# Optimization experiments

Measured on AMD Instinct MI355X. Metric: run time of the kernel, lower is better.

Reference implementation:

```python
import jax, jax.numpy as jnp
import numpy as np

T, D_IN, D_OUT, E = 8192, 1024, 1024, 8
LN_EPS = 1e-5


def setup_inputs() -> dict:
    key = jax.random.key(0)
    k1, k2, k3 = jax.random.split(key, 3)
    x = jax.random.normal(k1, (T, D_IN), dtype=jnp.float32)
    # tokens are pre-sorted by expert; equal load => capacity = T // E per expert
    expert_frequency = jnp.full((E,), T // E, dtype=jnp.int64)
    # per-expert Linear(input_dim, output_dim) params
    W = jax.random.normal(k2, (E, D_IN, D_OUT), dtype=jnp.float32) / np.sqrt(D_IN)
    b = jax.random.normal(k3, (E, D_OUT), dtype=jnp.float32) * 0.02
    # per-expert LayerNorm(output_dim) affine params
    ln_gamma = jnp.ones((E, D_OUT), dtype=jnp.float32)
    ln_beta = jnp.zeros((E, D_OUT), dtype=jnp.float32)
    return {
        "expert_ordered_input": x,
        "expert_frequency": expert_frequency,
        "W": W,
        "b": b,
        "ln_gamma": ln_gamma,
        "ln_beta": ln_beta,
    }


def reference(expert_ordered_input, expert_frequency, W, b, ln_gamma, ln_beta):
    # Grouped-GEMM form of: split tokens by expert_frequency, apply per-expert
    # LayerBlock (Linear -> relu -> LayerNorm), then concat along token dim.
    # Frequencies are equal (capacity = T // E), so the ragged split is a reshape.
    x = expert_ordered_input
    n_tok, d_in = x.shape
    n_exp = W.shape[0]
    cap = n_tok // n_exp  # static capacity per expert
    xe = x.reshape(n_exp, cap, d_in)                       # [E, cap, d_in]
    h = jnp.einsum("ecd,edf->ecf", xe, W) + b[:, None, :]  # [E, cap, d_out]
    h = jax.nn.relu(h)
    mu = jnp.mean(h, axis=-1, keepdims=True)
    var = jnp.var(h, axis=-1, keepdims=True)
    hn = (h - mu) * jax.lax.rsqrt(var + LN_EPS)
    out = hn * ln_gamma[:, None, :] + ln_beta[:, None, :]
    return out.reshape(n_tok, -1)                          # concat over experts
```

## Files before the change

### kernel.cpp

```cpp
#include <hip/hip_runtime.h>
#include <hip/hip_bf16.h>
#include <stdint.h>

#define T_TOK 8192
#define DIN   1024
#define DOUT  1024
#define NEXP  8
#define CAP   1024
#define LN_EPS 1e-5f

#define BM 256
#define BN 128
#define BKT 64
#define ABUF (BM * BKT)
#define BBUF (BN * BKT)
#define BUFSZ (ABUF + BBUF)

typedef __attribute__((ext_vector_type(8))) short short8;
typedef __attribute__((ext_vector_type(4))) float f32x4;

__device__ __forceinline__ unsigned short f2bf(float f) {
    union { float f; unsigned int u; } v; v.f = f;
    unsigned int u = v.u;
    unsigned int r = u + 0x7FFFu + ((u >> 16) & 1u);
    return (unsigned short)(r >> 16);
}
__device__ __forceinline__ float bf2f(unsigned short h) {
    union { unsigned int u; float f; } v; v.u = ((unsigned int)h) << 16;
    return v.f;
}

__device__ __forceinline__ void gld16(void* l, const void* g) {
    __builtin_amdgcn_global_load_lds(
        (const __attribute__((address_space(1))) unsigned int*)(uintptr_t)g,
        (__attribute__((address_space(3))) unsigned int*)(uintptr_t)l,
        16, 0, 0);
}

__global__ __launch_bounds__(256) void prep_kernel(
    const float* __restrict__ X, const float* __restrict__ W,
    unsigned short* __restrict__ Xb, unsigned short* __restrict__ Wt) {
    __shared__ float tile[64][65];
    int blk = blockIdx.x;
    int tid = threadIdx.x;
    if (blk < 1024) {
        int e  = blk & 7;
        int r0 = (blk >> 3) * 8;
        size_t base = ((size_t)(e * CAP + r0)) * 256 + tid;
#pragma unroll
        for (int q = 0; q < 8; q++) {
            size_t i = base + (size_t)q * 256;
            float4 v = ((const float4*)X)[i];
            ushort4 o;
            o.x = f2bf(v.x); o.y = f2bf(v.y); o.z = f2bf(v.z); o.w = f2bf(v.w);
            ((ushort4*)Xb)[i] = o;
        }
    } else {
        int t  = blk - 1024;
        int e  = t & 7;
        int tl = t >> 3;
        int k0 = (tl >> 4) * 64;
        int n0 = (tl & 15) * 64;
        const float* Wp = W + (size_t)e * DIN * DOUT;
        unsigned short* Wtp = Wt + (size_t)e * DIN * DOUT;
        int rr = tid >> 4;
        int cc = tid & 15;
#pragma unroll
        for (int q = 0; q < 4; q++) {
            int k = rr + q * 16;
            float4 v = *(const float4*)(Wp + (size_t)(k0 + k) * DOUT + n0 + cc * 4);
            tile[k][cc * 4 + 0] = v.x;
            tile[k][cc * 4 + 1] = v.y;
            tile[k][cc * 4 + 2] = v.z;
            tile[k][cc * 4 + 3] = v.w;
        }
        __syncthreads();
#pragma unroll
        for (int q = 0; q < 4; q++) {
            int n = rr + q * 16;
            ushort4 o;
            o.x = f2bf(tile[cc * 4 + 0][n]);
            o.y = f2bf(tile[cc * 4 + 1][n]);
            o.z = f2bf(tile[cc * 4 + 2][n]);
            o.w = f2bf(tile[cc * 4 + 3][n]);
            *(ushort4*)(Wtp + (size_t)(n0 + n) * DIN + k0 + cc * 4) = o;
        }
    }
}

__global__ __launch_bounds__(512, 2) void gemm7_kernel(
    const unsigned short* __restrict__ Xb,
    const unsigned short* __restrict__ Wt,
    const float* __restrict__ Bias,
    unsigned short* __restrict__ Hb,
    float2* __restrict__ P)
{
    __shared__ unsigned short lds[3 * BUFSZ];

    int blk = blockIdx.x;
    int e   = blk & 7;
    int ni  = (blk >> 3) & 7;
    int mi  = blk >> 6;
    int m0  = mi * BM;
    int n0  = ni * BN;

    int t    = threadIdx.x;
    int wave = t >> 6;
    int lane = t & 63;
    int wm   = (wave >> 1) * 64;
    int wn   = (wave & 1) * 64;
    int lrow = lane & 15;
    int quad = lane >> 4;
    int l7   = lrow & 7;

    const unsigned short* Ag = Xb + (size_t)(e * CAP + m0) * DIN;
    const unsigned short* Bg = Wt + (size_t)e * DOUT * DIN + (size_t)n0 * DIN;

    int trow   = t >> 3;
    int kg_src = (t & 7) ^ (trow & 7);

    int aoff0 = (wm + lrow) * BKT + ((quad) ^ l7) * 8;
    int aoff1 = (wm + lrow) * BKT + ((4 + quad) ^ l7) * 8;
    int boff0 = (wn + lrow) * BKT + ((quad) ^ l7) * 8;
    int boff1 = (wn + lrow) * BKT + ((4 + quad) ^ l7) * 8;

    f32x4 acc[4][4];
#pragma unroll
    for (int i = 0; i < 4; i++)
#pragma unroll
        for (int j = 0; j < 4; j++)
            acc[i][j] = (f32x4)(0.0f);

#define STAGE_H(bb, k0, h)                                                     \
    {                                                                          \
        unsigned short* Ab_ = &lds[(bb) * BUFSZ];                              \
        unsigned short* Bb_ = &lds[(bb) * BUFSZ + ABUF];                       \
        gld16(Ab_ + (((h) * 2 + 0) * 512 + t) * 8,                             \
              Ag + (size_t)(((h) * 2 + 0) * 64 + trow) * DIN + (k0) + kg_src * 8); \
        gld16(Ab_ + (((h) * 2 + 1) * 512 + t) * 8,                             \
              Ag + (size_t)(((h) * 2 + 1) * 64 + trow) * DIN + (k0) + kg_src * 8); \
        gld16(Bb_ + ((h) * 512 + t) * 8,                                       \
              Bg + (size_t)((h) * 64 + trow) * DIN + (k0) + kg_src * 8);       \
    }

#define LOADFRAGS(bb, ao, bo)                                                  \
    {                                                                          \
        const unsigned short* Ab_ = &lds[(bb) * BUFSZ];                        \
        const unsigned short* Bb_ = &lds[(bb) * BUFSZ + ABUF];                 \
        _Pragma("unroll")                                                      \
        for (int i = 0; i < 4; i++)                                            \
            af[i] = *(const short8*)&Ab_[(ao) + i * 16 * BKT];                 \
        _Pragma("unroll")                                                      \
        for (int j = 0; j < 4; j++)                                            \
            bf[j] = *(const short8*)&Bb_[(bo) + j * 16 * BKT];                 \
    }

#define MFMA16()                                                               \
    {                                                                          \
        __builtin_amdgcn_s_setprio(1);                                         \
        _Pragma("unroll")                                                      \
        for (int i = 0; i < 4; i++)                                            \
            _Pragma("unroll")                                                  \
            for (int j = 0; j < 4; j++)                                        \
                acc[i][j] = __builtin_amdgcn_mfma_f32_16x16x32_bf16(           \
                    af[i], bf[j], acc[i][j], 0, 0, 0);                         \
        __builtin_amdgcn_s_setprio(0);                                         \
    }

#define BAR() __builtin_amdgcn_s_barrier()
#define VMW(n) asm volatile("s_waitcnt vmcnt(" #n ")" ::: "memory")

    STAGE_H(0, 0, 0);
    STAGE_H(0, 0, 1);
    STAGE_H(1, BKT, 0);
    STAGE_H(1, BKT, 1);
    VMW(6);
    BAR();

    int cur = 0, nxt = 1, fut = 2;
    for (int p = 0; p < 14; ++p) {
        int k2 = (p + 2) * BKT;
        {
            short8 af[4], bf[4];
            LOADFRAGS(cur, aoff0, boff0);
            STAGE_H(fut, k2, 0);
            BAR();
            MFMA16();
            BAR();
        }
        {
            short8 af[4], bf[4];
            LOADFRAGS(cur, aoff1, boff1);
            STAGE_H(fut, k2, 1);
            BAR();
            MFMA16();
            VMW(6);
            BAR();
        }
        int tmp = cur; cur = nxt; nxt = fut; fut = tmp;
    }
    {
        short8 af[4], bf[4];
        LOADFRAGS(cur, aoff0, boff0);
        BAR(); MFMA16(); BAR();
    }
    {
        short8 af[4], bf[4];
        LOADFRAGS(cur, aoff1, boff1);
        BAR(); MFMA16();
        VMW(0);
        BAR();
    }
    {
        short8 af[4], bf[4];
        LOADFRAGS(nxt, aoff0, boff0);
        BAR(); MFMA16(); BAR();
    }
    {
        short8 af[4], bf[4];
        LOADFRAGS(nxt, aoff1, boff1);
        BAR(); MFMA16();
    }

#undef STAGE_H
#undef LOADFRAGS
#undef MFMA16
#undef BAR
#undef VMW

    asm volatile("" ::: "memory");

    float bias[4];
#pragma unroll
    for (int j = 0; j < 4; j++)
        bias[j] = Bias[e * DOUT + n0 + wn + j * 16 + lrow];

    int tok0  = e * CAP + m0 + wm;
    int chunk = ni * 2 + (wave & 1);

#pragma unroll
    for (int i = 0; i < 4; i++) {
#pragma unroll
        for (int r = 0; r < 4; r++) {
            float s = 0.f, ss = 0.f;
#pragma unroll
            for (int j = 0; j < 4; j++) {
                float v = fmaxf(acc[i][j][r] + bias[j], 0.f);
                acc[i][j][r] = v;
                s += v;
                ss = fmaf(v, v, ss);
            }
#pragma unroll
            for (int m = 1; m <= 8; m <<= 1) {
                s  += __shfl_xor(s, m);
                ss += __shfl_xor(ss, m);
            }
            int grow = tok0 + i * 16 + quad * 4 + r;
            if (lrow == 0)
                P[(size_t)grow * 16 + chunk] = make_float2(s, ss);
#pragma unroll
            for (int j = 0; j < 4; j++) {
                int gcol = n0 + wn + j * 16 + lrow;
                Hb[(size_t)grow * DOUT + gcol] = f2bf(acc[i][j][r]);
            }
        }
    }
}

__global__ __launch_bounds__(256) void ln2_kernel(
    const unsigned short* __restrict__ Hb,
    const float2* __restrict__ P,
    const float* __restrict__ G,
    const float* __restrict__ Bt,
    float* __restrict__ Out)
{
    int blk = blockIdx.x;
    int e   = blk & 7;
    int r8  = (blk >> 3) * 8;
    int row0 = e * CAP + r8;
    int tid = threadIdx.x;
    __shared__ float sh[8][2];

    if (tid < 128) {
        int r = tid >> 4;
        float2 p = P[(size_t)(row0 + r) * 16 + (tid & 15)];
        float s = p.x, ss = p.y;
#pragma unroll
        for (int m = 1; m <= 8; m <<= 1) {
            s  += __shfl_xor(s, m);
            ss += __shfl_xor(ss, m);
        }
        if ((tid & 15) == 0) {
            float mu  = s * (1.0f / DOUT);
            float var = fmaxf(ss * (1.0f / DOUT) - mu * mu, 0.f);
            sh[r][0] = mu;
            sh[r][1] = rsqrtf(var + LN_EPS);
        }
    }
    __syncthreads();

    float4 g = ((const float4*)G)[e * 256 + tid];
    float4 b = ((const float4*)Bt)[e * 256 + tid];
#pragma unroll
    for (int r = 0; r < 8; r++) {
        float mu = sh[r][0], rs = sh[r][1];
        ushort4 hb = ((const ushort4*)Hb)[(size_t)(row0 + r) * 256 + tid];
        float4 y;
        y.x = (bf2f(hb.x) - mu) * rs * g.x + b.x;
        y.y = (bf2f(hb.y) - mu) * rs * g.y + b.y;
        y.z = (bf2f(hb.z) - mu) * rs * g.z + b.z;
        y.w = (bf2f(hb.w) - mu) * rs * g.w + b.w;
        ((float4*)Out)[(size_t)(row0 + r) * 256 + tid] = y;
    }
}

extern "C" void kernel_launch(void* const* d_in, const int* in_sizes, int n_in,
                              void* d_out, int out_size, void* d_ws, size_t ws_size,
                              hipStream_t stream) {
    const float* x  = (const float*)d_in[0];
    const float* W  = (const float*)d_in[2];
    const float* b  = (const float*)d_in[3];
    const float* g  = (const float*)d_in[4];
    const float* be = (const float*)d_in[5];
    float* out = (float*)d_out;

    const size_t WT_BYTES = (size_t)NEXP * DIN * DOUT * 2;
    const size_t XB_BYTES = (size_t)T_TOK * DIN * 2;
    const size_t P_BYTES  = (size_t)T_TOK * 16 * 8;
    const size_t HB_BYTES = (size_t)T_TOK * DOUT * 2;
    if (ws_size < WT_BYTES + XB_BYTES + P_BYTES + HB_BYTES) return;

    unsigned short* Wt = (unsigned short*)d_ws;
    unsigned short* Xb = (unsigned short*)((char*)d_ws + WT_BYTES);
    float2* P = (float2*)((char*)d_ws + WT_BYTES + XB_BYTES);
    unsigned short* Hb = (unsigned short*)((char*)d_ws + WT_BYTES + XB_BYTES + P_BYTES);

    prep_kernel<<<dim3(3072), dim3(256), 0, stream>>>(x, W, Xb, Wt);
    gemm7_kernel<<<dim3(256), dim3(512), 0, stream>>>(Xb, Wt, b, Hb, P);
    ln2_kernel<<<dim3(1024), dim3(256), 0, stream>>>(Hb, P, g, be, out);
}
```

Measured before the change: 142.7 us.

## Fuse prep, GEMM and LayerNorm into one cooperative kernel with grid syncs

Merges the three launches (bf16 conversion/transpose, grouped GEMM, LayerNorm) into one cooperative kernel of 256 blocks, with grid-wide syncs between phases. The aim is to cut launch overhead and the inter-kernel gaps. The trade-off is that the prep and LN phases now run with only 256 blocks instead of 3072 and 1024, which lowers parallelism for those memory-bound phases, and each grid sync adds its own cost.

```diff
diff --git a/kernel.cpp b/kernel.cpp
--- a/kernel.cpp
+++ b/kernel.cpp
@@ -1,6 +1,9 @@
 #include <hip/hip_runtime.h>
+#include <hip/hip_cooperative_groups.h>
 #include <hip/hip_bf16.h>
 #include <stdint.h>
+
+namespace cg = cooperative_groups;
 
 #define T_TOK 8192
 #define DIN   1024
@@ -37,99 +40,102 @@
         16, 0, 0);
 }
 
-__global__ __launch_bounds__(256) void prep_kernel(
+__global__ __launch_bounds__(512, 2) void fused_kernel(
     const float* __restrict__ X, const float* __restrict__ W,
-    unsigned short* __restrict__ Xb, unsigned short* __restrict__ Wt) {
-    __shared__ float tile[64][65];
+    const float* __restrict__ Bias,
+    const float* __restrict__ G, const float* __restrict__ Bt,
+    float* __restrict__ Out,
+    unsigned short* __restrict__ Wt, unsigned short* __restrict__ Xb,
+    float2* __restrict__ P, unsigned short* __restrict__ Hb)
+{
+    __shared__ unsigned short lds[3 * BUFSZ];
+
     int blk = blockIdx.x;
-    int tid = threadIdx.x;
-    if (blk < 1024) {
-        int e  = blk & 7;
-        int r0 = (blk >> 3) * 8;
-        size_t base = ((size_t)(e * CAP + r0)) * 256 + tid;
-#pragma unroll
-        for (int q = 0; q < 8; q++) {
-            size_t i = base + (size_t)q * 256;
+    int e   = blk & 7;
+    int t   = threadIdx.x;
+
+    {
+        int r0   = (blk >> 3) * 32;
+        int rsub = t >> 8;
+        int c4   = t & 255;
+        size_t base = ((size_t)(e * CAP + r0 + rsub)) * 256 + c4;
+#pragma unroll
+        for (int q = 0; q < 16; q++) {
+            size_t i = base + (size_t)(q * 2) * 256;
             float4 v = ((const float4*)X)[i];
             ushort4 o;
             o.x = f2bf(v.x); o.y = f2bf(v.y); o.z = f2bf(v.z); o.w = f2bf(v.w);
             ((ushort4*)Xb)[i] = o;
         }
-    } else {
-        int t  = blk - 1024;
-        int e  = t & 7;
-        int tl = t >> 3;
-        int k0 = (tl >> 4) * 64;
-        int n0 = (tl & 15) * 64;
+    }
+    {
+        float (*tile)[65] = (float (*)[65])lds;
         const float* Wp = W + (size_t)e * DIN * DOUT;
         unsigned short* Wtp = Wt + (size_t)e * DIN * DOUT;
-        int rr = tid >> 4;
-        int cc = tid & 15;
-#pragma unroll
-        for (int q = 0; q < 4; q++) {
-            int k = rr + q * 16;
-            float4 v = *(const float4*)(Wp + (size_t)(k0 + k) * DOUT + n0 + cc * 4);
-            tile[k][cc * 4 + 0] = v.x;
-            tile[k][cc * 4 + 1] = v.y;
-            tile[k][cc * 4 + 2] = v.z;
-            tile[k][cc * 4 + 3] = v.w;
-        }
-        __syncthreads();
-#pragma unroll
-        for (int q = 0; q < 4; q++) {
-            int n = rr + q * 16;
-            ushort4 o;
-            o.x = f2bf(tile[cc * 4 + 0][n]);
-            o.y = f2bf(tile[cc * 4 + 1][n]);
-            o.z = f2bf(tile[cc * 4 + 2][n]);
-            o.w = f2bf(tile[cc * 4 + 3][n]);
-            *(ushort4*)(Wtp + (size_t)(n0 + n) * DIN + k0 + cc * 4) = o;
-        }
-    }
-}
-
-__global__ __launch_bounds__(512, 2) void gemm7_kernel(
-    const unsigned short* __restrict__ Xb,
-    const unsigned short* __restrict__ Wt,
-    const float* __restrict__ Bias,
-    unsigned short* __restrict__ Hb,
-    float2* __restrict__ P)
-{
-    __shared__ unsigned short lds[3 * BUFSZ];
-
-    int blk = blockIdx.x;
-    int e   = blk & 7;
-    int ni  = (blk >> 3) & 7;
-    int mi  = blk >> 6;
-    int m0  = mi * BM;
-    int n0  = ni * BN;
-
-    int t    = threadIdx.x;
-    int wave = t >> 6;
-    int lane = t & 63;
-    int wm   = (wave >> 1) * 64;
-    int wn   = (wave & 1) * 64;
-    int lrow = lane & 15;
-    int quad = lane >> 4;
-    int l7   = lrow & 7;
-
-    const unsigned short* Ag = Xb + (size_t)(e * CAP + m0) * DIN;
-    const unsigned short* Bg = Wt + (size_t)e * DOUT * DIN + (size_t)n0 * DIN;
-
-    int trow   = t >> 3;
-    int kg_src = (t & 7) ^ (trow & 7);
-
-    int aoff0 = (wm + lrow) * BKT + ((quad) ^ l7) * 8;
-    int aoff1 = (wm + lrow) * BKT + ((4 + quad) ^ l7) * 8;
-    int boff0 = (wn + lrow) * BKT + ((quad) ^ l7) * 8;
-    int boff1 = (wn + lrow) * BKT + ((4 + quad) ^ l7) * 8;
-
-    f32x4 acc[4][4];
-#pragma unroll
-    for (int i = 0; i < 4; i++)
-#pragma unroll
-        for (int j = 0; j < 4; j++)
-            acc[i][j] = (f32x4)(0.0f);
+        int tb = (blk >> 3) * 8;
+        int rr = t >> 4;
+        int cc = t & 15;
+        for (int i = 0; i < 8; i++) {
+            int tl = tb + i;
+            int k0 = (tl >> 4) * 64;
+            int n0 = (tl & 15) * 64;
+            __syncthreads();
+#pragma unroll
+            for (int q = 0; q < 2; q++) {
+                int k = rr + q * 32;
+                float4 v = *(const float4*)(Wp + (size_t)(k0 + k) * DOUT + n0 + cc * 4);
+                tile[k][cc * 4 + 0] = v.x;
+                tile[k][cc * 4 + 1] = v.y;
+                tile[k][cc * 4 + 2] = v.z;
+                tile[k][cc * 4 + 3] = v.w;
+            }
+            __syncthreads();
+#pragma unroll
+            for (int q = 0; q < 2; q++) {
+                int n = rr + q * 32;
+                ushort4 o;
+                o.x = f2bf(tile[cc * 4 + 0][n]);
+                o.y = f2bf(tile[cc * 4 + 1][n]);
+                o.z = f2bf(tile[cc * 4 + 2][n]);
+                o.w = f2bf(tile[cc * 4 + 3][n]);
+                *(ushort4*)(Wtp + (size_t)(n0 + n) * DIN + k0 + cc * 4) = o;
+            }
+        }
+    }
+
+    cg::this_grid().sync();
+
+    {
+        int ni  = (blk >> 3) & 7;
+        int mi  = blk >> 6;
+        int m0  = mi * BM;
+        int n0  = ni * BN;
+
+        int wave = t >> 6;
+        int lane = t & 63;
+        int wm   = (wave >> 1) * 64;
+        int wn   = (wave & 1) * 64;
+        int lrow = lane & 15;
+        int quad = lane >> 4;
+        int l7   = lrow & 7;
+
+        const unsigned short* Ag = Xb + (size_t)(e * CAP + m0) * DIN;
+        const unsigned short* Bg = Wt + (size_t)e * DOUT * DIN + (size_t)n0 * DIN;
+
+        int trow   = t >> 3;
+        int kg_src = (t & 7) ^ (trow & 7);
+
+        int aoff0 = (wm + lrow) * BKT + ((quad) ^ l7) * 8;
+        int aoff1 = (wm + lrow) * BKT + ((4 + quad) ^ l7) * 8;
+        int boff0 = (wn + lrow) * BKT + ((quad) ^ l7) * 8;
+        int boff1 = (wn + lrow) * BKT + ((4 + quad) ^ l7) * 8;
+
+        f32x4 acc[4][4];
+#pragma unroll
+        for (int i = 0; i < 4; i++)
+#pragma unroll
+            for (int j = 0; j < 4; j++)
+                acc[i][j] = (f32x4)(0.0f);
 
 #define STAGE_H(bb, k0, h)                                                     \
     {                                                                          \
@@ -170,57 +176,57 @@
 #define BAR() __builtin_amdgcn_s_barrier()
 #define VMW(n) asm volatile("s_waitcnt vmcnt(" #n ")" ::: "memory")
 
-    STAGE_H(0, 0, 0);
-    STAGE_H(0, 0, 1);
-    STAGE_H(1, BKT, 0);
-    STAGE_H(1, BKT, 1);
-    VMW(6);
-    BAR();
-
-    int cur = 0, nxt = 1, fut = 2;
-    for (int p = 0; p < 14; ++p) {
-        int k2 = (p + 2) * BKT;
+        STAGE_H(0, 0, 0);
+        STAGE_H(0, 0, 1);
+        STAGE_H(1, BKT, 0);
+        STAGE_H(1, BKT, 1);
+        VMW(6);
+        BAR();
+
+        int cur = 0, nxt = 1, fut = 2;
+        for (int p = 0; p < 14; ++p) {
+            int k2 = (p + 2) * BKT;
+            {
+                short8 af[4], bf[4];
+                LOADFRAGS(cur, aoff0, boff0);
+                STAGE_H(fut, k2, 0);
+                BAR();
+                MFMA16();
+                BAR();
+            }
+            {
+                short8 af[4], bf[4];
+                LOADFRAGS(cur, aoff1, boff1);
+                STAGE_H(fut, k2, 1);
+                BAR();
+                MFMA16();
+                VMW(6);
+                BAR();
+            }
+            int tmp = cur; cur = nxt; nxt = fut; fut = tmp;
+        }
         {
             short8 af[4], bf[4];
             LOADFRAGS(cur, aoff0, boff0);
-            STAGE_H(fut, k2, 0);
-            BAR();
-            MFMA16();
-            BAR();
+            BAR(); MFMA16(); BAR();
         }
         {
             short8 af[4], bf[4];
             LOADFRAGS(cur, aoff1, boff1);
-            STAGE_H(fut, k2, 1);
+            BAR(); MFMA16();
+            VMW(0);
             BAR();
-            MFMA16();
-            VMW(6);
-            BAR();
-        }
-        int tmp = cur; cur = nxt; nxt = fut; fut = tmp;
-    }
-    {
-        short8 af[4], bf[4];
-        LOADFRAGS(cur, aoff0, boff0);
-        BAR(); MFMA16(); BAR();
-    }
-    {
-        short8 af[4], bf[4];
-        LOADFRAGS(cur, aoff1, boff1);
-        BAR(); MFMA16();
-        VMW(0);
-        BAR();
-    }
-    {
-        short8 af[4], bf[4];
-        LOADFRAGS(nxt, aoff0, boff0);
-        BAR(); MFMA16(); BAR();
-    }
-    {
-        short8 af[4], bf[4];
-        LOADFRAGS(nxt, aoff1, boff1);
-        BAR(); MFMA16();
-    }
+        }
+        {
+            short8 af[4], bf[4];
+            LOADFRAGS(nxt, aoff0, boff0);
+            BAR(); MFMA16(); BAR();
+        }
+        {
+            short8 af[4], bf[4];
+            LOADFRAGS(nxt, aoff1, boff1);
+            BAR(); MFMA16();
+        }
 
 #undef STAGE_H
 #undef LOADFRAGS
@@ -228,89 +234,86 @@
 #undef BAR
 #undef VMW
 
-    asm volatile("" ::: "memory");
-
-    float bias[4];
-#pragma unroll
-    for (int j = 0; j < 4; j++)
-        bias[j] = Bias[e * DOUT + n0 + wn + j * 16 + lrow];
-
-    int tok0  = e * CAP + m0 + wm;
-    int chunk = ni * 2 + (wave & 1);
-
-#pragma unroll
-    for (int i = 0; i < 4; i++) {
-#pragma unroll
-        for (int r = 0; r < 4; r++) {
-            float s = 0.f, ss = 0.f;
-#pragma unroll
-            for (int j = 0; j < 4; j++) {
-                float v = fmaxf(acc[i][j][r] + bias[j], 0.f);
-                acc[i][j][r] = v;
-                s += v;
-                ss = fmaf(v, v, ss);
-            }
+        asm volatile("" ::: "memory");
+
+        float bias[4];
+#pragma unroll
+        for (int j = 0; j < 4; j++)
+            bias[j] = Bias[e * DOUT + n0 + wn + j * 16 + lrow];
+
+        int tok0  = e * CAP + m0 + wm;
+        int chunk = ni * 2 + (wave & 1);
+
+#pragma unroll
+        for (int i = 0; i < 4; i++) {
+#pragma unroll
+            for (int r = 0; r < 4; r++) {
+                float s = 0.f, ss = 0.f;
+#pragma unroll
+                for (int j = 0; j < 4; j++) {
+                    float v = fmaxf(acc[i][j][r] + bias[j], 0.f);
+                    acc[i][j][r] = v;
+                    s += v;
+                    ss = fmaf(v, v, ss);
+                }
+#pragma unroll
+                for (int m = 1; m <= 8; m <<= 1) {
+                    s  += __shfl_xor(s, m);
+                    ss += __shfl_xor(ss, m);
+                }
+                int grow = tok0 + i * 16 + quad * 4 + r;
+                if (lrow == 0)
+                    P[(size_t)grow * 16 + chunk] = make_float2(s, ss);
+#pragma unroll
+                for (int j = 0; j < 4; j++) {
+                    int gcol = n0 + wn + j * 16 + lrow;
+                    Hb[(size_t)grow * DOUT + gcol] = f2bf(acc[i][j][r]);
+                }
+            }
+        }
+    }
+
+    cg::this_grid().sync();
+
+    {
+        int r0   = (blk >> 3) * 32;
+        int row0 = e * CAP + r0;
+        float* shf = (float*)lds;
+
+        {
+            int r = t >> 4;
+            float2 p = P[(size_t)(row0 + r) * 16 + (t & 15)];
+            float s = p.x, ss = p.y;
 #pragma unroll
             for (int m = 1; m <= 8; m <<= 1) {
                 s  += __shfl_xor(s, m);
                 ss += __shfl_xor(ss, m);
             }
-            int grow = tok0 + i * 16 + quad * 4 + r;
-            if (lrow == 0)
-                P[(size_t)grow * 16 + chunk] = make_float2(s, ss);
-#pragma unroll
-            for (int j = 0; j < 4; j++) {
-                int gcol = n0 + wn + j * 16 + lrow;
-                Hb[(size_t)grow * DOUT + gcol] = f2bf(acc[i][j][r]);
-            }
-        }
-    }
-}
-
-__global__ __launch_bounds__(256) void ln2_kernel(
-    const unsigned short* __restrict__ Hb,
-    const float2* __restrict__ P,
-    const float* __restrict__ G,
-    const float* __restrict__ Bt,
-    float* __restrict__ Out)
-{
-    int blk = blockIdx.x;
-    int e   = blk & 7;
-    int r8  = (blk >> 3) * 8;
-    int row0 = e * CAP + r8;
-    int tid = threadIdx.x;
-    __shared__ float sh[8][2];
-
-    if (tid < 128) {
-        int r = tid >> 4;
-        float2 p = P[(size_t)(row0 + r) * 16 + (tid & 15)];
-        float s = p.x, ss = p.y;
-#pragma unroll
-        for (int m = 1; m <= 8; m <<= 1) {
-            s  += __shfl_xor(s, m);
-            ss += __shfl_xor(ss, m);
-        }
-        if ((tid & 15) == 0) {
-            float mu  = s * (1.0f / DOUT);
-            float var = fmaxf(ss * (1.0f / DOUT) - mu * mu, 0.f);
-            sh[r][0] = mu;
-            sh[r][1] = rsqrtf(var + LN_EPS);
-        }
-    }
-    __syncthreads();
-
-    float4 g = ((const float4*)G)[e * 256 + tid];
-    float4 b = ((const float4*)Bt)[e * 256 + tid];
-#pragma unroll
-    for (int r = 0; r < 8; r++) {
-        float mu = sh[r][0], rs = sh[r][1];
-        ushort4 hb = ((const ushort4*)Hb)[(size_t)(row0 + r) * 256 + tid];
-        float4 y;
-        y.x = (bf2f(hb.x) - mu) * rs * g.x + b.x;
-        y.y = (bf2f(hb.y) - mu) * rs * g.y + b.y;
-        y.z = (bf2f(hb.z) - mu) * rs * g.z + b.z;
-        y.w = (bf2f(hb.w) - mu) * rs * g.w + b.w;
-        ((float4*)Out)[(size_t)(row0 + r) * 256 + tid] = y;
+            if ((t & 15) == 0) {
+                float mu  = s * (1.0f / DOUT);
+                float var = fmaxf(ss * (1.0f / DOUT) - mu * mu, 0.f);
+                shf[r * 2 + 0] = mu;
+                shf[r * 2 + 1] = rsqrtf(var + LN_EPS);
+            }
+        }
+        __syncthreads();
+
+        int rsub = t >> 8;
+        int c4   = t & 255;
+        float4 g = ((const float4*)G)[e * 256 + c4];
+        float4 b = ((const float4*)Bt)[e * 256 + c4];
+#pragma unroll
+        for (int q = 0; q < 16; q++) {
+            int r = q * 2 + rsub;
+            float mu = shf[r * 2 + 0], rs = shf[r * 2 + 1];
+            ushort4 hb = ((const ushort4*)Hb)[(size_t)(row0 + r) * 256 + c4];
+            float4 y;
+            y.x = (bf2f(hb.x) - mu) * rs * g.x + b.x;
+            y.y = (bf2f(hb.y) - mu) * rs * g.y + b.y;
+            y.z = (bf2f(hb.z) - mu) * rs * g.z + b.z;
+            y.w = (bf2f(hb.w) - mu) * rs * g.w + b.w;
+            ((float4*)Out)[(size_t)(row0 + r) * 256 + c4] = y;
+        }
     }
 }
 
@@ -335,7 +338,8 @@
     float2* P = (float2*)((char*)d_ws + WT_BYTES + XB_BYTES);
     unsigned short* Hb = (unsigned short*)((char*)d_ws + WT_BYTES + XB_BYTES + P_BYTES);
 
-    prep_kernel<<<dim3(3072), dim3(256), 0, stream>>>(x, W, Xb, Wt);
-    gemm7_kernel<<<dim3(256), dim3(512), 0, stream>>>(Xb, Wt, b, Hb, P);
-    ln2_kernel<<<dim3(1024), dim3(256), 0, stream>>>(Hb, P, g, be, out);
-}
+    void* args[] = {(void*)&x, (void*)&W, (void*)&b, (void*)&g, (void*)&be,
+                    (void*)&out, (void*)&Wt, (void*)&Xb, (void*)&P, (void*)&Hb};
+    hipLaunchCooperativeKernel((const void*)fused_kernel,
+                               dim3(256), dim3(512), args, 0, stream);
+}
```

Result: slower. 229.5 us (+60.9%).
